# Performance work log

Measured on AMD Instinct MI355X. Metric: run time of the kernel, lower is better.

## Reference

```python
import jax, jax.numpy as jnp
import numpy as np

N_NODES = 100000
N_EDGES = 1600000
IN_DIM = 128
OUT_DIM = 128


def setup_inputs() -> dict:
    key = jax.random.key(0)
    k1, k2, k3, k4, k5 = jax.random.split(key, 5)
    x = jax.random.normal(k1, (N_NODES, IN_DIM), dtype=jnp.float32)
    edge_src = jax.random.randint(k2, (N_EDGES,), 0, N_NODES, dtype=jnp.int32)
    edge_dst = jax.random.randint(k3, (N_EDGES,), 0, N_NODES, dtype=jnp.int32)
    # nn.Linear(in_dim*2, out_dim): W stored here as [2*in_dim, out_dim] (already transposed)
    W = jax.random.normal(k4, (2 * IN_DIM, OUT_DIM), dtype=jnp.float32) * (1.0 / np.sqrt(2 * IN_DIM))
    b = jax.random.normal(k5, (OUT_DIM,), dtype=jnp.float32) * 0.01
    return {"x": x, "edge_src": edge_src, "edge_dst": edge_dst, "W": W, "b": b}


def reference(x, edge_src, edge_dst, W, b):
    # adj_mean @ x  ==  mean over neighbors: sum_j x[src_j] into row dst_j, / deg(dst)
    n = x.shape[0]
    deg = jax.ops.segment_sum(jnp.ones_like(edge_dst, dtype=x.dtype), edge_dst, num_segments=n)
    deg = jnp.maximum(deg, 1.0)  # rows with no neighbors -> zero vector (0/1)
    neigh = jax.ops.segment_sum(x[edge_src], edge_dst, num_segments=n) / deg[:, None]
    # concat([x, neigh], dim=1) then Linear
    out = jnp.concatenate([x, neigh], axis=1) @ W + b
    return out
```

## Files before the change

### kernel.cpp

```cpp
#include <hip/hip_runtime.h>

#define IN_DIM 128
#define OUT_DIM 128
#define PADCAP 1792
#define EPB 8192

typedef short bf16x8 __attribute__((ext_vector_type(8)));
typedef float f32x4 __attribute__((ext_vector_type(4)));
typedef float f32x2 __attribute__((ext_vector_type(2)));
typedef unsigned int u32x4 __attribute__((ext_vector_type(4)));

__device__ __forceinline__ unsigned short f2bf(float f) {
    union { float f; unsigned int u; } v; v.f = f;
    unsigned int u = v.u;
    u += 0x7FFFu + ((u >> 16) & 1u);
    return (unsigned short)(u >> 16);
}

__global__ __launch_bounds__(256) void prep_kernel(const float* __restrict__ x,
                                                   unsigned char* __restrict__ xq,
                                                   const float* __restrict__ W,
                                                   unsigned short* __restrict__ WF,
                                                   int* __restrict__ cursor,
                                                   int nN, int total8, int nconv, int nb) {
    const int b = blockIdx.x;
    const int t = threadIdx.x;
    if (b < nconv) {
        int i = b * 256 + t;
        if (i >= total8) return;
        const float4* p = (const float4*)x + (size_t)i * 2;
        float4 v0 = p[0], v1 = p[1];
        int w0 = 0, w1 = 0;
        w0 = __builtin_amdgcn_cvt_pk_fp8_f32(v0.x, v0.y, w0, false);
        w0 = __builtin_amdgcn_cvt_pk_fp8_f32(v0.z, v0.w, w0, true);
        w1 = __builtin_amdgcn_cvt_pk_fp8_f32(v1.x, v1.y, w1, false);
        w1 = __builtin_amdgcn_cvt_pk_fp8_f32(v1.z, v1.w, w1, true);
        uint2 o; o.x = (unsigned int)w0; o.y = (unsigned int)w1;
        int node = i >> 4, oct = i & 15;
        int h = oct >> 3, o8 = oct & 7;
        *(uint2*)(xq + (size_t)h * (nN + 1) * 64 + (size_t)node * 64 + o8 * 8) = o;
    } else if (b < nconv + 16) {
        int tt = (b - nconv) * 256 + t;
        int frag = tt >> 6, lane = tt & 63;
        int f = frag >> 3, c = frag & 7;
        int col = c * 16 + (lane & 15);
        int kbase = f * 32 + (lane >> 4) * 8;
        bf16x8 h;
#pragma unroll
        for (int i = 0; i < 8; i++)
            h[i] = (short)f2bf(W[(size_t)(kbase + i) * OUT_DIM + col]);
        *(bf16x8*)(WF + (size_t)tt * 8) = h;
    } else if (b == nconv + 16) {
        if (t < 32) {
            int h = t >> 4, o = t & 15;
            *(unsigned int*)(xq + (size_t)h * (nN + 1) * 64 + (size_t)nN * 64 + o * 4) = 0u;
        }
    } else {
        int i = (b - nconv - 17) * 256 + t;
        if (i < nb) cursor[i] = i * PADCAP;
    }
}

__global__ __launch_bounds__(1024) void place_kernel(const int* __restrict__ src,
                                                     const int* __restrict__ dst,
                                                     int* __restrict__ cursor,
                                                     unsigned int* __restrict__ csr_packed,
                                                     int nE, int nb) {
    __shared__ int lcnt[2048];
    __shared__ int lbase[2048];
    const int t = threadIdx.x;
    for (int i = t; i < nb; i += 1024) lcnt[i] = 0;
    __syncthreads();
    const int e0 = blockIdx.x * EPB;
    unsigned int meta[EPB / 1024];
#pragma unroll
    for (int k = 0; k < EPB / 1024; k++) {
        int e = e0 + k * 1024 + t;
        if (e < nE) {
            int d = dst[e];
            int bk = d >> 6, dl = d & 63;
            int r = atomicAdd(&lcnt[bk], 1);
            meta[k] = ((unsigned)bk << 20) | ((unsigned)dl << 14) | (unsigned)r;
        } else meta[k] = 0xFFFFFFFFu;
    }
    __syncthreads();
    for (int i = t; i < nb; i += 1024) {
        int c = lcnt[i];
        lbase[i] = c ? atomicAdd(&cursor[i], c) : 0;
    }
    __syncthreads();
#pragma unroll
    for (int k = 0; k < EPB / 1024; k++) {
        if (meta[k] != 0xFFFFFFFFu) {
            int e = e0 + k * 1024 + t;
            unsigned int m = meta[k];
            int bk = m >> 20, dl = (m >> 14) & 63, r = m & 0x3FFF;
            csr_packed[lbase[bk] + r] = ((unsigned)dl << 17) | (unsigned)src[e];
        }
    }
}

__global__ __launch_bounds__(256, 4) void qgather_kernel(const unsigned char* __restrict__ xq,
                                                         const unsigned int* __restrict__ csr_packed,
                                                         const int* __restrict__ cursor,
                                                         unsigned short* __restrict__ neigh,
                                                         int nN, int nb) {
    __shared__ unsigned int el[PADCAP];
    __shared__ int bcnt[64];
    __shared__ int bpst[64];
    __shared__ int bst[64];
    __shared__ int bdg[64];
    __shared__ int brw[64];

    const int bid = blockIdx.x;
    const int xcd = bid & 7;
    const int half = xcd & 1;
    const int bucket = (bid >> 3) * 4 + (xcd >> 1);
    if (bucket >= nb) return;

    const int t = threadIdx.x;
    const int lane = t & 63;
    const int wave = t >> 6;

    const size_t e0 = (size_t)bucket * PADCAP;
    int n = cursor[bucket] - bucket * PADCAP;
    if (n > PADCAP) n = PADCAP;

    const unsigned int sentinel = (unsigned)nN << 6;
    if (t < 64) bcnt[t] = 0;
#pragma unroll
    for (int k = 0; k < 7; k++) el[k * 256 + t] = sentinel;
    __syncthreads();

    unsigned int pk[7]; int rk[7];
#pragma unroll
    for (int k = 0; k < 7; k++) {
        int idx = k * 256 + t;
        if (idx < n) {
            unsigned int p = csr_packed[e0 + idx];
            pk[k] = p;
            rk[k] = atomicAdd(&bcnt[(p >> 17) & 63], 1);
        } else pk[k] = 0xFFFFFFFFu;
    }
    __syncthreads();

    if (wave == 0) {
        int dg = bcnt[lane];
        int pl = (dg + 7) & ~7;
        int s = pl;
#pragma unroll
        for (int off = 1; off < 64; off <<= 1) {
            int u = __shfl_up(s, off);
            if (lane >= off) s += u;
        }
        bpst[lane] = s - pl;
        unsigned key = ((unsigned)dg << 6) | (unsigned)lane;
#pragma unroll
        for (int k = 2; k <= 64; k <<= 1) {
#pragma unroll
            for (int j = k >> 1; j > 0; j >>= 1) {
                unsigned other = __shfl_xor(key, j);
                bool lower = (lane & j) == 0;
                bool asc   = (lane & k) == 0;
                unsigned mn = min(key, other), mx = max(key, other);
                key = (lower == asc) ? mn : mx;
            }
        }
        int rowid = key & 63;
        bst[lane] = bpst[rowid];
        bdg[lane] = (int)(key >> 6);
        brw[lane] = rowid;
    }
    __syncthreads();

#pragma unroll
    for (int k = 0; k < 7; k++) {
        if (pk[k] != 0xFFFFFFFFu) {
            int dl = (pk[k] >> 17) & 63;
            el[bpst[dl] + rk[k]] = (pk[k] & 0x1FFFFu) << 6;
        }
    }
    __syncthreads();

    const int g = lane >> 2;
    const int c = lane & 3;
    const unsigned char* plane = xq + (size_t)half * (nN + 1) * 64 + c * 16;
    const int hoff = half * 64;

    const int r  = wave * 16 + g;
    const int st = bst[r];
    const int dg = bdg[r];
    const int pl = (dg + 7) & ~7;
    const unsigned int* ep = el + st;

    f32x2 a0{0.f,0.f}, a1{0.f,0.f}, a2{0.f,0.f}, a3{0.f,0.f},
          a4{0.f,0.f}, a5{0.f,0.f}, a6{0.f,0.f}, a7{0.f,0.f};
    for (int j = 0; j < pl; j += 8) {
        const unsigned int s0 = ep[j + ((0 + g) & 7)];
        const unsigned int s1 = ep[j + ((1 + g) & 7)];
        const unsigned int s2 = ep[j + ((2 + g) & 7)];
        const unsigned int s3 = ep[j + ((3 + g) & 7)];
        const unsigned int s4 = ep[j + ((4 + g) & 7)];
        const unsigned int s5 = ep[j + ((5 + g) & 7)];
        const unsigned int s6 = ep[j + ((6 + g) & 7)];
        const unsigned int s7 = ep[j + ((7 + g) & 7)];
        const uint4 v0 = *(const uint4*)(plane + s0);
        const uint4 v1 = *(const uint4*)(plane + s1);
        const uint4 v2 = *(const uint4*)(plane + s2);
        const uint4 v3 = *(const uint4*)(plane + s3);
        const uint4 v4 = *(const uint4*)(plane + s4);
        const uint4 v5 = *(const uint4*)(plane + s5);
        const uint4 v6 = *(const uint4*)(plane + s6);
        const uint4 v7 = *(const uint4*)(plane + s7);
        f32x2 p;
        p = __builtin_amdgcn_cvt_pk_f32_fp8(v0.x, false); a0 += p;
        p = __builtin_amdgcn_cvt_pk_f32_fp8(v0.x, true);  a1 += p;
        p = __builtin_amdgcn_cvt_pk_f32_fp8(v0.y, false); a2 += p;
        p = __builtin_amdgcn_cvt_pk_f32_fp8(v0.y, true);  a3 += p;
        p = __builtin_amdgcn_cvt_pk_f32_fp8(v0.z, false); a4 += p;
        p = __builtin_amdgcn_cvt_pk_f32_fp8(v0.z, true);  a5 += p;
        p = __builtin_amdgcn_cvt_pk_f32_fp8(v0.w, false); a6 += p;
        p = __builtin_amdgcn_cvt_pk_f32_fp8(v0.w, true);  a7 += p;
        p = __builtin_amdgcn_cvt_pk_f32_fp8(v1.x, false); a0 += p;
        p = __builtin_amdgcn_cvt_pk_f32_fp8(v1.x, true);  a1 += p;
        p = __builtin_amdgcn_cvt_pk_f32_fp8(v1.y, false); a2 += p;
        p = __builtin_amdgcn_cvt_pk_f32_fp8(v1.y, true);  a3 += p;
        p = __builtin_amdgcn_cvt_pk_f32_fp8(v1.z, false); a4 += p;
        p = __builtin_amdgcn_cvt_pk_f32_fp8(v1.z, true);  a5 += p;
        p = __builtin_amdgcn_cvt_pk_f32_fp8(v1.w, false); a6 += p;
        p = __builtin_amdgcn_cvt_pk_f32_fp8(v1.w, true);  a7 += p;
        p = __builtin_amdgcn_cvt_pk_f32_fp8(v2.x, false); a0 += p;
        p = __builtin_amdgcn_cvt_pk_f32_fp8(v2.x, true);  a1 += p;
        p = __builtin_amdgcn_cvt_pk_f32_fp8(v2.y, false); a2 += p;
        p = __builtin_amdgcn_cvt_pk_f32_fp8(v2.y, true);  a3 += p;
        p = __builtin_amdgcn_cvt_pk_f32_fp8(v2.z, false); a4 += p;
        p = __builtin_amdgcn_cvt_pk_f32_fp8(v2.z, true);  a5 += p;
        p = __builtin_amdgcn_cvt_pk_f32_fp8(v2.w, false); a6 += p;
        p = __builtin_amdgcn_cvt_pk_f32_fp8(v2.w, true);  a7 += p;
        p = __builtin_amdgcn_cvt_pk_f32_fp8(v3.x, false); a0 += p;
        p = __builtin_amdgcn_cvt_pk_f32_fp8(v3.x, true);  a1 += p;
        p = __builtin_amdgcn_cvt_pk_f32_fp8(v3.y, false); a2 += p;
        p = __builtin_amdgcn_cvt_pk_f32_fp8(v3.y, true);  a3 += p;
        p = __builtin_amdgcn_cvt_pk_f32_fp8(v3.z, false); a4 += p;
        p = __builtin_amdgcn_cvt_pk_f32_fp8(v3.z, true);  a5 += p;
        p = __builtin_amdgcn_cvt_pk_f32_fp8(v3.w, false); a6 += p;
        p = __builtin_amdgcn_cvt_pk_f32_fp8(v3.w, true);  a7 += p;
        p = __builtin_amdgcn_cvt_pk_f32_fp8(v4.x, false); a0 += p;
        p = __builtin_amdgcn_cvt_pk_f32_fp8(v4.x, true);  a1 += p;
        p = __builtin_amdgcn_cvt_pk_f32_fp8(v4.y, false); a2 += p;
        p = __builtin_amdgcn_cvt_pk_f32_fp8(v4.y, true);  a3 += p;
        p = __builtin_amdgcn_cvt_pk_f32_fp8(v4.z, false); a4 += p;
        p = __builtin_amdgcn_cvt_pk_f32_fp8(v4.z, true);  a5 += p;
        p = __builtin_amdgcn_cvt_pk_f32_fp8(v4.w, false); a6 += p;
        p = __builtin_amdgcn_cvt_pk_f32_fp8(v4.w, true);  a7 += p;
        p = __builtin_amdgcn_cvt_pk_f32_fp8(v5.x, false); a0 += p;
        p = __builtin_amdgcn_cvt_pk_f32_fp8(v5.x, true);  a1 += p;
        p = __builtin_amdgcn_cvt_pk_f32_fp8(v5.y, false); a2 += p;
        p = __builtin_amdgcn_cvt_pk_f32_fp8(v5.y, true);  a3 += p;
        p = __builtin_amdgcn_cvt_pk_f32_fp8(v5.z, false); a4 += p;
        p = __builtin_amdgcn_cvt_pk_f32_fp8(v5.z, true);  a5 += p;
        p = __builtin_amdgcn_cvt_pk_f32_fp8(v5.w, false); a6 += p;
        p = __builtin_amdgcn_cvt_pk_f32_fp8(v5.w, true);  a7 += p;
        p = __builtin_amdgcn_cvt_pk_f32_fp8(v6.x, false); a0 += p;
        p = __builtin_amdgcn_cvt_pk_f32_fp8(v6.x, true);  a1 += p;
        p = __builtin_amdgcn_cvt_pk_f32_fp8(v6.y, false); a2 += p;
        p = __builtin_amdgcn_cvt_pk_f32_fp8(v6.y, true);  a3 += p;
        p = __builtin_amdgcn_cvt_pk_f32_fp8(v6.z, false); a4 += p;
        p = __builtin_amdgcn_cvt_pk_f32_fp8(v6.z, true);  a5 += p;
        p = __builtin_amdgcn_cvt_pk_f32_fp8(v6.w, false); a6 += p;
        p = __builtin_amdgcn_cvt_pk_f32_fp8(v6.w, true);  a7 += p;
        p = __builtin_amdgcn_cvt_pk_f32_fp8(v7.x, false); a0 += p;
        p = __builtin_amdgcn_cvt_pk_f32_fp8(v7.x, true);  a1 += p;
        p = __builtin_amdgcn_cvt_pk_f32_fp8(v7.y, false); a2 += p;
        p = __builtin_amdgcn_cvt_pk_f32_fp8(v7.y, true);  a3 += p;
        p = __builtin_amdgcn_cvt_pk_f32_fp8(v7.z, false); a4 += p;
        p = __builtin_amdgcn_cvt_pk_f32_fp8(v7.z, true);  a5 += p;
        p = __builtin_amdgcn_cvt_pk_f32_fp8(v7.w, false); a6 += p;
        p = __builtin_amdgcn_cvt_pk_f32_fp8(v7.w, true);  a7 += p;
    }
    const float rd = 1.0f / (float)((dg > 0) ? dg : 1);
    a0 *= rd; a1 *= rd; a2 *= rd; a3 *= rd;
    a4 *= rd; a5 *= rd; a6 *= rd; a7 *= rd;
    unsigned int w0, w1, w2, w3, w4, w5, w6, w7;
    asm("v_cvt_pk_bf16_f32 %0, %1, %2" : "=v"(w0) : "v"(a0.x), "v"(a0.y));
    asm("v_cvt_pk_bf16_f32 %0, %1, %2" : "=v"(w1) : "v"(a1.x), "v"(a1.y));
    asm("v_cvt_pk_bf16_f32 %0, %1, %2" : "=v"(w2) : "v"(a2.x), "v"(a2.y));
    asm("v_cvt_pk_bf16_f32 %0, %1, %2" : "=v"(w3) : "v"(a3.x), "v"(a3.y));
    asm("v_cvt_pk_bf16_f32 %0, %1, %2" : "=v"(w4) : "v"(a4.x), "v"(a4.y));
    asm("v_cvt_pk_bf16_f32 %0, %1, %2" : "=v"(w5) : "v"(a5.x), "v"(a5.y));
    asm("v_cvt_pk_bf16_f32 %0, %1, %2" : "=v"(w6) : "v"(a6.x), "v"(a6.y));
    asm("v_cvt_pk_bf16_f32 %0, %1, %2" : "=v"(w7) : "v"(a7.x), "v"(a7.y));
    const int row = bucket * 64 + brw[r];
    unsigned short* np = neigh + (size_t)row * IN_DIM + hoff + c * 16;
    u32x4 olo = {w0, w1, w2, w3};
    u32x4 ohi = {w4, w5, w6, w7};
    *(u32x4*)np = olo;
    *(u32x4*)(np + 8) = ohi;
}

__global__ __launch_bounds__(256, 6) void gemm_kernel(const float* __restrict__ x,
                                                      const unsigned short* __restrict__ neigh,
                                                      const unsigned short* __restrict__ WF,
                                                      const float* __restrict__ bias,
                                                      float* __restrict__ out, int nN) {
    const int t = threadIdx.x;
    const int lane = t & 63;
    const int wave = t >> 6;
    const int row0 = blockIdx.x * 64;

    f32x4 acc[8];
#pragma unroll
    for (int c = 0; c < 8; c++) acc[c] = f32x4{0.f, 0.f, 0.f, 0.f};

    const int arow = wave * 16 + (lane & 15);
    const int koff = (lane >> 4) * 8;
    const int rowc = min(row0 + arow, nN - 1);
    const float*          xrow = x     + (size_t)rowc * IN_DIM;
    const unsigned short* nrow = neigh + (size_t)rowc * IN_DIM;

#pragma unroll
    for (int f = 0; f < 8; f++) {
        bf16x8 af;
        if (f < 4) {
            const float* px = xrow + f * 32 + koff;
            float4 v0 = *(const float4*)px;
            float4 v1 = *(const float4*)(px + 4);
            unsigned int r0, r1, r2, r3;
            asm("v_cvt_pk_bf16_f32 %0, %1, %2" : "=v"(r0) : "v"(v0.x), "v"(v0.y));
            asm("v_cvt_pk_bf16_f32 %0, %1, %2" : "=v"(r1) : "v"(v0.z), "v"(v0.w));
            asm("v_cvt_pk_bf16_f32 %0, %1, %2" : "=v"(r2) : "v"(v1.x), "v"(v1.y));
            asm("v_cvt_pk_bf16_f32 %0, %1, %2" : "=v"(r3) : "v"(v1.z), "v"(v1.w));
            union { unsigned int u[4]; bf16x8 v; } cv;
            cv.u[0] = r0; cv.u[1] = r1; cv.u[2] = r2; cv.u[3] = r3;
            af = cv.v;
        } else {
            af = *(const bf16x8*)(nrow + (f - 4) * 32 + koff);
        }
#pragma unroll
        for (int c = 0; c < 8; c++) {
            bf16x8 bf = *(const bf16x8*)(WF + ((size_t)(f * 8 + c) * 64 + lane) * 8);
            acc[c] = __builtin_amdgcn_mfma_f32_16x16x32_bf16(af, bf, acc[c], 0, 0, 0);
        }
    }

    const int orow0 = row0 + wave * 16 + (lane >> 4) * 4;
    const int ocol  = lane & 15;
#pragma unroll
    for (int c = 0; c < 8; c++) {
        const float bv = bias[c * 16 + ocol];
#pragma unroll
        for (int r = 0; r < 4; r++) {
            int row = orow0 + r;
            if (row < nN)
                out[(size_t)row * OUT_DIM + c * 16 + ocol] = acc[c][r] + bv;
        }
    }
}

extern "C" void kernel_launch(void* const* d_in, const int* in_sizes, int n_in,
                              void* d_out, int out_size, void* d_ws, size_t ws_size,
                              hipStream_t stream) {
    const float* x        = (const float*)d_in[0];
    const int*   edge_src = (const int*)d_in[1];
    const int*   edge_dst = (const int*)d_in[2];
    const float* W        = (const float*)d_in[3];
    const float* bias     = (const float*)d_in[4];
    float* out = (float*)d_out;

    const int nN = in_sizes[0] / IN_DIM;
    const int nE = in_sizes[1];
    const int nb = (nN + 63) >> 6;

    int* cursor = (int*)d_ws;
    unsigned int* csr_packed = (unsigned int*)(cursor + 2048);
    unsigned char* xq = (unsigned char*)(csr_packed + (size_t)nb * PADCAP);
    unsigned short* WF = (unsigned short*)(xq + (size_t)2 * (nN + 1) * 64);
    unsigned short* neigh = WF + 128 * 256;

    const int total8 = nN * IN_DIM / 8;
    const int nconv  = (total8 + 255) / 256;
    const int ninit  = (nb + 255) / 256;
    prep_kernel<<<nconv + 17 + ninit, 256, 0, stream>>>(x, xq, W, WF, cursor,
                                                        nN, total8, nconv, nb);

    const int eblk = (nE + EPB - 1) / EPB;
    place_kernel<<<eblk, 1024, 0, stream>>>(edge_src, edge_dst, cursor, csr_packed, nE, nb);

    const int nbp4 = (nb + 3) / 4;
    qgather_kernel<<<nbp4 * 8, 256, 0, stream>>>(xq, csr_packed, cursor, neigh, nN, nb);
    gemm_kernel<<<(nN + 63) / 64, 256, 0, stream>>>(x, neigh, WF, bias, out, nN);
}
```

Baseline: 101.9 us.

## Fuse neighbor gather into GEMM kernel via shared-memory tile

Merges the fp8 gather/mean kernel and the MFMA GEMM into one kernel per 64-node bucket. The aggregated neighbor rows go into an LDS tile instead of a global bf16 buffer, which removes one launch and a global write plus read of the neigh array. The fp8 copy of x becomes a single 128-byte row layout instead of two 64-byte half-planes, and each block now gathers full rows itself, so the XCD-split half-plane scheduling is dropped. In exchange the block uses more LDS and registers, and gather and GEMM phases can no longer overlap across separate kernels, which may reduce occupancy and parallelism.

```diff
diff --git a/kernel.cpp b/kernel.cpp
--- a/kernel.cpp
+++ b/kernel.cpp
@@ -36,9 +36,7 @@
         w1 = __builtin_amdgcn_cvt_pk_fp8_f32(v1.x, v1.y, w1, false);
         w1 = __builtin_amdgcn_cvt_pk_fp8_f32(v1.z, v1.w, w1, true);
         uint2 o; o.x = (unsigned int)w0; o.y = (unsigned int)w1;
-        int node = i >> 4, oct = i & 15;
-        int h = oct >> 3, o8 = oct & 7;
-        *(uint2*)(xq + (size_t)h * (nN + 1) * 64 + (size_t)node * 64 + o8 * 8) = o;
+        *(uint2*)(xq + (size_t)i * 8) = o;
     } else if (b < nconv + 16) {
         int tt = (b - nconv) * 256 + t;
         int frag = tt >> 6, lane = tt & 63;
@@ -51,10 +49,8 @@
             h[i] = (short)f2bf(W[(size_t)(kbase + i) * OUT_DIM + col]);
         *(bf16x8*)(WF + (size_t)tt * 8) = h;
     } else if (b == nconv + 16) {
-        if (t < 32) {
-            int h = t >> 4, o = t & 15;
-            *(unsigned int*)(xq + (size_t)h * (nN + 1) * 64 + (size_t)nN * 64 + o * 4) = 0u;
-        }
+        if (t < 32)
+            *(unsigned int*)(xq + (size_t)nN * 128 + t * 4) = 0u;
     } else {
         int i = (b - nconv - 17) * 256 + t;
         if (i < nb) cursor[i] = i * PADCAP;
@@ -100,24 +96,22 @@
     }
 }
 
-__global__ __launch_bounds__(256, 4) void qgather_kernel(const unsigned char* __restrict__ xq,
-                                                         const unsigned int* __restrict__ csr_packed,
-                                                         const int* __restrict__ cursor,
-                                                         unsigned short* __restrict__ neigh,
-                                                         int nN, int nb) {
+__global__ __launch_bounds__(256, 4) void fused_kernel(const unsigned char* __restrict__ xq,
+                                                       const unsigned int* __restrict__ csr_packed,
+                                                       const int* __restrict__ cursor,
+                                                       const unsigned short* __restrict__ WF,
+                                                       const float* __restrict__ x,
+                                                       const float* __restrict__ bias,
+                                                       float* __restrict__ out, int nN) {
     __shared__ unsigned int el[PADCAP];
+    __shared__ __align__(16) short Ntile[64 * 136];
     __shared__ int bcnt[64];
     __shared__ int bpst[64];
     __shared__ int bst[64];
     __shared__ int bdg[64];
     __shared__ int brw[64];
 
-    const int bid = blockIdx.x;
-    const int xcd = bid & 7;
-    const int half = xcd & 1;
-    const int bucket = (bid >> 3) * 4 + (xcd >> 1);
-    if (bucket >= nb) return;
-
+    const int bucket = blockIdx.x;
     const int t = threadIdx.x;
     const int lane = t & 63;
     const int wave = t >> 6;
@@ -126,7 +120,7 @@
     int n = cursor[bucket] - bucket * PADCAP;
     if (n > PADCAP) n = PADCAP;
 
-    const unsigned int sentinel = (unsigned)nN << 6;
+    const unsigned int sentinel = (unsigned)nN << 7;
     if (t < 64) bcnt[t] = 0;
 #pragma unroll
     for (int k = 0; k < 7; k++) el[k * 256 + t] = sentinel;
@@ -177,136 +171,128 @@
     for (int k = 0; k < 7; k++) {
         if (pk[k] != 0xFFFFFFFFu) {
             int dl = (pk[k] >> 17) & 63;
-            el[bpst[dl] + rk[k]] = (pk[k] & 0x1FFFFu) << 6;
-        }
-    }
-    __syncthreads();
-
-    const int g = lane >> 2;
-    const int c = lane & 3;
-    const unsigned char* plane = xq + (size_t)half * (nN + 1) * 64 + c * 16;
-    const int hoff = half * 64;
-
-    const int r  = wave * 16 + g;
-    const int st = bst[r];
-    const int dg = bdg[r];
-    const int pl = (dg + 7) & ~7;
-    const unsigned int* ep = el + st;
-
-    f32x2 a0{0.f,0.f}, a1{0.f,0.f}, a2{0.f,0.f}, a3{0.f,0.f},
-          a4{0.f,0.f}, a5{0.f,0.f}, a6{0.f,0.f}, a7{0.f,0.f};
-    for (int j = 0; j < pl; j += 8) {
-        const unsigned int s0 = ep[j + ((0 + g) & 7)];
-        const unsigned int s1 = ep[j + ((1 + g) & 7)];
-        const unsigned int s2 = ep[j + ((2 + g) & 7)];
-        const unsigned int s3 = ep[j + ((3 + g) & 7)];
-        const unsigned int s4 = ep[j + ((4 + g) & 7)];
-        const unsigned int s5 = ep[j + ((5 + g) & 7)];
-        const unsigned int s6 = ep[j + ((6 + g) & 7)];
-        const unsigned int s7 = ep[j + ((7 + g) & 7)];
-        const uint4 v0 = *(const uint4*)(plane + s0);
-        const uint4 v1 = *(const uint4*)(plane + s1);
-        const uint4 v2 = *(const uint4*)(plane + s2);
-        const uint4 v3 = *(const uint4*)(plane + s3);
-        const uint4 v4 = *(const uint4*)(plane + s4);
-        const uint4 v5 = *(const uint4*)(plane + s5);
-        const uint4 v6 = *(const uint4*)(plane + s6);
-        const uint4 v7 = *(const uint4*)(plane + s7);
-        f32x2 p;
-        p = __builtin_amdgcn_cvt_pk_f32_fp8(v0.x, false); a0 += p;
-        p = __builtin_amdgcn_cvt_pk_f32_fp8(v0.x, true);  a1 += p;
-        p = __builtin_amdgcn_cvt_pk_f32_fp8(v0.y, false); a2 += p;
-        p = __builtin_amdgcn_cvt_pk_f32_fp8(v0.y, true);  a3 += p;
-        p = __builtin_amdgcn_cvt_pk_f32_fp8(v0.z, false); a4 += p;
-        p = __builtin_amdgcn_cvt_pk_f32_fp8(v0.z, true);  a5 += p;
-        p = __builtin_amdgcn_cvt_pk_f32_fp8(v0.w, false); a6 += p;
-        p = __builtin_amdgcn_cvt_pk_f32_fp8(v0.w, true);  a7 += p;
-        p = __builtin_amdgcn_cvt_pk_f32_fp8(v1.x, false); a0 += p;
-        p = __builtin_amdgcn_cvt_pk_f32_fp8(v1.x, true);  a1 += p;
-        p = __builtin_amdgcn_cvt_pk_f32_fp8(v1.y, false); a2 += p;
-        p = __builtin_amdgcn_cvt_pk_f32_fp8(v1.y, true);  a3 += p;
-        p = __builtin_amdgcn_cvt_pk_f32_fp8(v1.z, false); a4 += p;
-        p = __builtin_amdgcn_cvt_pk_f32_fp8(v1.z, true);  a5 += p;
-        p = __builtin_amdgcn_cvt_pk_f32_fp8(v1.w, false); a6 += p;
-        p = __builtin_amdgcn_cvt_pk_f32_fp8(v1.w, true);  a7 += p;
-        p = __builtin_amdgcn_cvt_pk_f32_fp8(v2.x, false); a0 += p;
-        p = __builtin_amdgcn_cvt_pk_f32_fp8(v2.x, true);  a1 += p;
-        p = __builtin_amdgcn_cvt_pk_f32_fp8(v2.y, false); a2 += p;
-        p = __builtin_amdgcn_cvt_pk_f32_fp8(v2.y, true);  a3 += p;
-        p = __builtin_amdgcn_cvt_pk_f32_fp8(v2.z, false); a4 += p;
-        p = __builtin_amdgcn_cvt_pk_f32_fp8(v2.z, true);  a5 += p;
-        p = __builtin_amdgcn_cvt_pk_f32_fp8(v2.w, false); a6 += p;
-        p = __builtin_amdgcn_cvt_pk_f32_fp8(v2.w, true);  a7 += p;
-        p = __builtin_amdgcn_cvt_pk_f32_fp8(v3.x, false); a0 += p;
-        p = __builtin_amdgcn_cvt_pk_f32_fp8(v3.x, true);  a1 += p;
-        p = __builtin_amdgcn_cvt_pk_f32_fp8(v3.y, false); a2 += p;
-        p = __builtin_amdgcn_cvt_pk_f32_fp8(v3.y, true);  a3 += p;
-        p = __builtin_amdgcn_cvt_pk_f32_fp8(v3.z, false); a4 += p;
-        p = __builtin_amdgcn_cvt_pk_f32_fp8(v3.z, true);  a5 += p;
-        p = __builtin_amdgcn_cvt_pk_f32_fp8(v3.w, false); a6 += p;
-        p = __builtin_amdgcn_cvt_pk_f32_fp8(v3.w, true);  a7 += p;
-        p = __builtin_amdgcn_cvt_pk_f32_fp8(v4.x, false); a0 += p;
-        p = __builtin_amdgcn_cvt_pk_f32_fp8(v4.x, true);  a1 += p;
-        p = __builtin_amdgcn_cvt_pk_f32_fp8(v4.y, false); a2 += p;
-        p = __builtin_amdgcn_cvt_pk_f32_fp8(v4.y, true);  a3 += p;
-        p = __builtin_amdgcn_cvt_pk_f32_fp8(v4.z, false); a4 += p;
-        p = __builtin_amdgcn_cvt_pk_f32_fp8(v4.z, true);  a5 += p;
-        p = __builtin_amdgcn_cvt_pk_f32_fp8(v4.w, false); a6 += p;
-        p = __builtin_amdgcn_cvt_pk_f32_fp8(v4.w, true);  a7 += p;
-        p = __builtin_amdgcn_cvt_pk_f32_fp8(v5.x, false); a0 += p;
-        p = __builtin_amdgcn_cvt_pk_f32_fp8(v5.x, true);  a1 += p;
-        p = __builtin_amdgcn_cvt_pk_f32_fp8(v5.y, false); a2 += p;
-        p = __builtin_amdgcn_cvt_pk_f32_fp8(v5.y, true);  a3 += p;
-        p = __builtin_amdgcn_cvt_pk_f32_fp8(v5.z, false); a4 += p;
-        p = __builtin_amdgcn_cvt_pk_f32_fp8(v5.z, true);  a5 += p;
-        p = __builtin_amdgcn_cvt_pk_f32_fp8(v5.w, false); a6 += p;
-        p = __builtin_amdgcn_cvt_pk_f32_fp8(v5.w, true);  a7 += p;
-        p = __builtin_amdgcn_cvt_pk_f32_fp8(v6.x, false); a0 += p;
-        p = __builtin_amdgcn_cvt_pk_f32_fp8(v6.x, true);  a1 += p;
-        p = __builtin_amdgcn_cvt_pk_f32_fp8(v6.y, false); a2 += p;
-        p = __builtin_amdgcn_cvt_pk_f32_fp8(v6.y, true);  a3 += p;
-        p = __builtin_amdgcn_cvt_pk_f32_fp8(v6.z, false); a4 += p;
-        p = __builtin_amdgcn_cvt_pk_f32_fp8(v6.z, true);  a5 += p;
-        p = __builtin_amdgcn_cvt_pk_f32_fp8(v6.w, false); a6 += p;
-        p = __builtin_amdgcn_cvt_pk_f32_fp8(v6.w, true);  a7 += p;
-        p = __builtin_amdgcn_cvt_pk_f32_fp8(v7.x, false); a0 += p;
-        p = __builtin_amdgcn_cvt_pk_f32_fp8(v7.x, true);  a1 += p;
-        p = __builtin_amdgcn_cvt_pk_f32_fp8(v7.y, false); a2 += p;
-        p = __builtin_amdgcn_cvt_pk_f32_fp8(v7.y, true);  a3 += p;
-        p = __builtin_amdgcn_cvt_pk_f32_fp8(v7.z, false); a4 += p;
-        p = __builtin_amdgcn_cvt_pk_f32_fp8(v7.z, true);  a5 += p;
-        p = __builtin_amdgcn_cvt_pk_f32_fp8(v7.w, false); a6 += p;
-        p = __builtin_amdgcn_cvt_pk_f32_fp8(v7.w, true);  a7 += p;
-    }
-    const float rd = 1.0f / (float)((dg > 0) ? dg : 1);
-    a0 *= rd; a1 *= rd; a2 *= rd; a3 *= rd;
-    a4 *= rd; a5 *= rd; a6 *= rd; a7 *= rd;
-    unsigned int w0, w1, w2, w3, w4, w5, w6, w7;
-    asm("v_cvt_pk_bf16_f32 %0, %1, %2" : "=v"(w0) : "v"(a0.x), "v"(a0.y));
-    asm("v_cvt_pk_bf16_f32 %0, %1, %2" : "=v"(w1) : "v"(a1.x), "v"(a1.y));
-    asm("v_cvt_pk_bf16_f32 %0, %1, %2" : "=v"(w2) : "v"(a2.x), "v"(a2.y));
-    asm("v_cvt_pk_bf16_f32 %0, %1, %2" : "=v"(w3) : "v"(a3.x), "v"(a3.y));
-    asm("v_cvt_pk_bf16_f32 %0, %1, %2" : "=v"(w4) : "v"(a4.x), "v"(a4.y));
-    asm("v_cvt_pk_bf16_f32 %0, %1, %2" : "=v"(w5) : "v"(a5.x), "v"(a5.y));
-    asm("v_cvt_pk_bf16_f32 %0, %1, %2" : "=v"(w6) : "v"(a6.x), "v"(a6.y));
-    asm("v_cvt_pk_bf16_f32 %0, %1, %2" : "=v"(w7) : "v"(a7.x), "v"(a7.y));
-    const int row = bucket * 64 + brw[r];
-    unsigned short* np = neigh + (size_t)row * IN_DIM + hoff + c * 16;
-    u32x4 olo = {w0, w1, w2, w3};
-    u32x4 ohi = {w4, w5, w6, w7};
-    *(u32x4*)np = olo;
-    *(u32x4*)(np + 8) = ohi;
-}
-
-__global__ __launch_bounds__(256, 6) void gemm_kernel(const float* __restrict__ x,
-                                                      const unsigned short* __restrict__ neigh,
-                                                      const unsigned short* __restrict__ WF,
-                                                      const float* __restrict__ bias,
-                                                      float* __restrict__ out, int nN) {
-    const int t = threadIdx.x;
-    const int lane = t & 63;
-    const int wave = t >> 6;
-    const int row0 = blockIdx.x * 64;
+            el[bpst[dl] + rk[k]] = (pk[k] & 0x1FFFFu) << 7;
+        }
+    }
+    __syncthreads();
+
+    {
+        const int g = lane >> 3;
+        const int c = lane & 7;
+        const unsigned char* plane = xq + c * 16;
+#pragma unroll
+        for (int set = 0; set < 2; set++) {
+            const int r  = wave * 16 + set * 8 + g;
+            const int st = bst[r];
+            const int dg = bdg[r];
+            const int pl = (dg + 7) & ~7;
+            const unsigned int* ep = el + st;
+
+            f32x2 a0{0.f,0.f}, a1{0.f,0.f}, a2{0.f,0.f}, a3{0.f,0.f},
+                  a4{0.f,0.f}, a5{0.f,0.f}, a6{0.f,0.f}, a7{0.f,0.f};
+            for (int j = 0; j < pl; j += 8) {
+                const unsigned int s0 = ep[j + ((0 + g) & 7)];
+                const unsigned int s1 = ep[j + ((1 + g) & 7)];
+                const unsigned int s2 = ep[j + ((2 + g) & 7)];
+                const unsigned int s3 = ep[j + ((3 + g) & 7)];
+                const unsigned int s4 = ep[j + ((4 + g) & 7)];
+                const unsigned int s5 = ep[j + ((5 + g) & 7)];
+                const unsigned int s6 = ep[j + ((6 + g) & 7)];
+                const unsigned int s7 = ep[j + ((7 + g) & 7)];
+                const uint4 v0 = *(const uint4*)(plane + s0);
+                const uint4 v1 = *(const uint4*)(plane + s1);
+                const uint4 v2 = *(const uint4*)(plane + s2);
+                const uint4 v3 = *(const uint4*)(plane + s3);
+                const uint4 v4 = *(const uint4*)(plane + s4);
+                const uint4 v5 = *(const uint4*)(plane + s5);
+                const uint4 v6 = *(const uint4*)(plane + s6);
+                const uint4 v7 = *(const uint4*)(plane + s7);
+                f32x2 p;
+                p = __builtin_amdgcn_cvt_pk_f32_fp8(v0.x, false); a0 += p;
+                p = __builtin_amdgcn_cvt_pk_f32_fp8(v0.x, true);  a1 += p;
+                p = __builtin_amdgcn_cvt_pk_f32_fp8(v0.y, false); a2 += p;
+                p = __builtin_amdgcn_cvt_pk_f32_fp8(v0.y, true);  a3 += p;
+                p = __builtin_amdgcn_cvt_pk_f32_fp8(v0.z, false); a4 += p;
+                p = __builtin_amdgcn_cvt_pk_f32_fp8(v0.z, true);  a5 += p;
+                p = __builtin_amdgcn_cvt_pk_f32_fp8(v0.w, false); a6 += p;
+                p = __builtin_amdgcn_cvt_pk_f32_fp8(v0.w, true);  a7 += p;
+                p = __builtin_amdgcn_cvt_pk_f32_fp8(v1.x, false); a0 += p;
+                p = __builtin_amdgcn_cvt_pk_f32_fp8(v1.x, true);  a1 += p;
+                p = __builtin_amdgcn_cvt_pk_f32_fp8(v1.y, false); a2 += p;
+                p = __builtin_amdgcn_cvt_pk_f32_fp8(v1.y, true);  a3 += p;
+                p = __builtin_amdgcn_cvt_pk_f32_fp8(v1.z, false); a4 += p;
+                p = __builtin_amdgcn_cvt_pk_f32_fp8(v1.z, true);  a5 += p;
+                p = __builtin_amdgcn_cvt_pk_f32_fp8(v1.w, false); a6 += p;
+                p = __builtin_amdgcn_cvt_pk_f32_fp8(v1.w, true);  a7 += p;
+                p = __builtin_amdgcn_cvt_pk_f32_fp8(v2.x, false); a0 += p;
+                p = __builtin_amdgcn_cvt_pk_f32_fp8(v2.x, true);  a1 += p;
+                p = __builtin_amdgcn_cvt_pk_f32_fp8(v2.y, false); a2 += p;
+                p = __builtin_amdgcn_cvt_pk_f32_fp8(v2.y, true);  a3 += p;
+                p = __builtin_amdgcn_cvt_pk_f32_fp8(v2.z, false); a4 += p;
+                p = __builtin_amdgcn_cvt_pk_f32_fp8(v2.z, true);  a5 += p;
+                p = __builtin_amdgcn_cvt_pk_f32_fp8(v2.w, false); a6 += p;
+                p = __builtin_amdgcn_cvt_pk_f32_fp8(v2.w, true);  a7 += p;
+                p = __builtin_amdgcn_cvt_pk_f32_fp8(v3.x, false); a0 += p;
+                p = __builtin_amdgcn_cvt_pk_f32_fp8(v3.x, true);  a1 += p;
+                p = __builtin_amdgcn_cvt_pk_f32_fp8(v3.y, false); a2 += p;
+                p = __builtin_amdgcn_cvt_pk_f32_fp8(v3.y, true);  a3 += p;
+                p = __builtin_amdgcn_cvt_pk_f32_fp8(v3.z, false); a4 += p;
+                p = __builtin_amdgcn_cvt_pk_f32_fp8(v3.z, true);  a5 += p;
+                p = __builtin_amdgcn_cvt_pk_f32_fp8(v3.w, false); a6 += p;
+                p = __builtin_amdgcn_cvt_pk_f32_fp8(v3.w, true);  a7 += p;
+                p = __builtin_amdgcn_cvt_pk_f32_fp8(v4.x, false); a0 += p;
+                p = __builtin_amdgcn_cvt_pk_f32_fp8(v4.x, true);  a1 += p;
+                p = __builtin_amdgcn_cvt_pk_f32_fp8(v4.y, false); a2 += p;
+                p = __builtin_amdgcn_cvt_pk_f32_fp8(v4.y, true);  a3 += p;
+                p = __builtin_amdgcn_cvt_pk_f32_fp8(v4.z, false); a4 += p;
+                p = __builtin_amdgcn_cvt_pk_f32_fp8(v4.z, true);  a5 += p;
+                p = __builtin_amdgcn_cvt_pk_f32_fp8(v4.w, false); a6 += p;
+                p = __builtin_amdgcn_cvt_pk_f32_fp8(v4.w, true);  a7 += p;
+                p = __builtin_amdgcn_cvt_pk_f32_fp8(v5.x, false); a0 += p;
+                p = __builtin_amdgcn_cvt_pk_f32_fp8(v5.x, true);  a1 += p;
+                p = __builtin_amdgcn_cvt_pk_f32_fp8(v5.y, false); a2 += p;
+                p = __builtin_amdgcn_cvt_pk_f32_fp8(v5.y, true);  a3 += p;
+                p = __builtin_amdgcn_cvt_pk_f32_fp8(v5.z, false); a4 += p;
+                p = __builtin_amdgcn_cvt_pk_f32_fp8(v5.z, true);  a5 += p;
+                p = __builtin_amdgcn_cvt_pk_f32_fp8(v5.w, false); a6 += p;
+                p = __builtin_amdgcn_cvt_pk_f32_fp8(v5.w, true);  a7 += p;
+                p = __builtin_amdgcn_cvt_pk_f32_fp8(v6.x, false); a0 += p;
+                p = __builtin_amdgcn_cvt_pk_f32_fp8(v6.x, true);  a1 += p;
+                p = __builtin_amdgcn_cvt_pk_f32_fp8(v6.y, false); a2 += p;
+                p = __builtin_amdgcn_cvt_pk_f32_fp8(v6.y, true);  a3 += p;
+                p = __builtin_amdgcn_cvt_pk_f32_fp8(v6.z, false); a4 += p;
+                p = __builtin_amdgcn_cvt_pk_f32_fp8(v6.z, true);  a5 += p;
+                p = __builtin_amdgcn_cvt_pk_f32_fp8(v6.w, false); a6 += p;
+                p = __builtin_amdgcn_cvt_pk_f32_fp8(v6.w, true);  a7 += p;
+                p = __builtin_amdgcn_cvt_pk_f32_fp8(v7.x, false); a0 += p;
+                p = __builtin_amdgcn_cvt_pk_f32_fp8(v7.x, true);  a1 += p;
+                p = __builtin_amdgcn_cvt_pk_f32_fp8(v7.y, false); a2 += p;
+                p = __builtin_amdgcn_cvt_pk_f32_fp8(v7.y, true);  a3 += p;
+                p = __builtin_amdgcn_cvt_pk_f32_fp8(v7.z, false); a4 += p;
+                p = __builtin_amdgcn_cvt_pk_f32_fp8(v7.z, true);  a5 += p;
+                p = __builtin_amdgcn_cvt_pk_f32_fp8(v7.w, false); a6 += p;
+                p = __builtin_amdgcn_cvt_pk_f32_fp8(v7.w, true);  a7 += p;
+            }
+            const float rd = 1.0f / (float)((dg > 0) ? dg : 1);
+            a0 *= rd; a1 *= rd; a2 *= rd; a3 *= rd;
+            a4 *= rd; a5 *= rd; a6 *= rd; a7 *= rd;
+            unsigned int w0, w1, w2, w3, w4, w5, w6, w7;
+            asm("v_cvt_pk_bf16_f32 %0, %1, %2" : "=v"(w0) : "v"(a0.x), "v"(a0.y));
+            asm("v_cvt_pk_bf16_f32 %0, %1, %2" : "=v"(w1) : "v"(a1.x), "v"(a1.y));
+            asm("v_cvt_pk_bf16_f32 %0, %1, %2" : "=v"(w2) : "v"(a2.x), "v"(a2.y));
+            asm("v_cvt_pk_bf16_f32 %0, %1, %2" : "=v"(w3) : "v"(a3.x), "v"(a3.y));
+            asm("v_cvt_pk_bf16_f32 %0, %1, %2" : "=v"(w4) : "v"(a4.x), "v"(a4.y));
+            asm("v_cvt_pk_bf16_f32 %0, %1, %2" : "=v"(w5) : "v"(a5.x), "v"(a5.y));
+            asm("v_cvt_pk_bf16_f32 %0, %1, %2" : "=v"(w6) : "v"(a6.x), "v"(a6.y));
+            asm("v_cvt_pk_bf16_f32 %0, %1, %2" : "=v"(w7) : "v"(a7.x), "v"(a7.y));
+            short* np = &Ntile[brw[r] * 136 + c * 16];
+            u32x4 olo = {w0, w1, w2, w3};
+            u32x4 ohi = {w4, w5, w6, w7};
+            *(u32x4*)np = olo;
+            *(u32x4*)(np + 8) = ohi;
+        }
+    }
+    __syncthreads();
 
     f32x4 acc[8];
 #pragma unroll
@@ -314,9 +300,8 @@
 
     const int arow = wave * 16 + (lane & 15);
     const int koff = (lane >> 4) * 8;
-    const int rowc = min(row0 + arow, nN - 1);
-    const float*          xrow = x     + (size_t)rowc * IN_DIM;
-    const unsigned short* nrow = neigh + (size_t)rowc * IN_DIM;
+    const int rowc = min(bucket * 64 + arow, nN - 1);
+    const float* xrow = x + (size_t)rowc * IN_DIM;
 
 #pragma unroll
     for (int f = 0; f < 8; f++) {
@@ -334,7 +319,7 @@
             cv.u[0] = r0; cv.u[1] = r1; cv.u[2] = r2; cv.u[3] = r3;
             af = cv.v;
         } else {
-            af = *(const bf16x8*)(nrow + (f - 4) * 32 + koff);
+            af = *(const bf16x8*)&Ntile[arow * 136 + (f - 4) * 32 + koff];
         }
 #pragma unroll
         for (int c = 0; c < 8; c++) {
@@ -343,7 +328,7 @@
         }
     }
 
-    const int orow0 = row0 + wave * 16 + (lane >> 4) * 4;
+    const int orow0 = bucket * 64 + wave * 16 + (lane >> 4) * 4;
     const int ocol  = lane & 15;
 #pragma unroll
     for (int c = 0; c < 8; c++) {
@@ -374,8 +359,7 @@
     int* cursor = (int*)d_ws;
     unsigned int* csr_packed = (unsigned int*)(cursor + 2048);
     unsigned char* xq = (unsigned char*)(csr_packed + (size_t)nb * PADCAP);
-    unsigned short* WF = (unsigned short*)(xq + (size_t)2 * (nN + 1) * 64);
-    unsigned short* neigh = WF + 128 * 256;
+    unsigned short* WF = (unsigned short*)(xq + (size_t)(nN + 1) * 128);
 
     const int total8 = nN * IN_DIM / 8;
     const int nconv  = (total8 + 255) / 256;
@@ -386,7 +370,5 @@
     const int eblk = (nE + EPB - 1) / EPB;
     place_kernel<<<eblk, 1024, 0, stream>>>(edge_src, edge_dst, cursor, csr_packed, nE, nb);
 
-    const int nbp4 = (nb + 3) / 4;
-    qgather_kernel<<<nbp4 * 8, 256, 0, stream>>>(xq, csr_packed, cursor, neigh, nN, nb);
-    gemm_kernel<<<(nN + 63) / 64, 256, 0, stream>>>(x, neigh, WF, bias, out, nN);
-}
+    fused_kernel<<<nb, 256, 0, stream>>>(xq, csr_packed, cursor, WF, x, bias, out, nN);
+}
```

After: 94.96 us. -6.8%, faster.
